# Kernel tuning notes

Hardware: AMD Instinct MI355X
Metric: run time of the kernel (lower is better)

Reference implementation:

```python
import jax, jax.numpy as jnp
import numpy as np

BS, QLEN, DIM, NH = 4, 2048, 1024, 16
DH = DIM // NH
NEG = float(np.finfo(np.float32).min)


def setup_inputs() -> dict:
    key = jax.random.key(0)
    ks = jax.random.split(key, 10)
    s = 1.0 / np.sqrt(DIM)
    return {
        "hidden_states": jax.random.normal(ks[0], (BS, QLEN, DIM), jnp.float32),
        "attention_mask": jnp.ones((BS, QLEN), jnp.int32),
        "Wq": jax.random.normal(ks[1], (DIM, DIM), jnp.float32) * s,
        "bq": jnp.zeros((DIM,), jnp.float32),
        "Wk": jax.random.normal(ks[2], (DIM, DIM), jnp.float32) * s,
        "bk": jnp.zeros((DIM,), jnp.float32),
        "Wv": jax.random.normal(ks[3], (DIM, DIM), jnp.float32) * s,
        "bv": jnp.zeros((DIM,), jnp.float32),
        "Wo": jax.random.normal(ks[4], (DIM, DIM), jnp.float32) * s,
        "bo": jnp.zeros((DIM,), jnp.float32),
    }


def _heads(x, bs):
    # [bs, len, dim] -> [bs, n_heads, len, dim_per_head]
    return x.reshape(bs, -1, NH, DH).transpose(0, 2, 1, 3)


def reference(hidden_states, attention_mask, Wq, bq, Wk, bk, Wv, bv, Wo, bo):
    bs, qlen, dim = hidden_states.shape
    q = _heads(hidden_states @ Wq.T + bq, bs) / jnp.sqrt(jnp.asarray(DH, hidden_states.dtype))
    k = _heads(hidden_states @ Wk.T + bk, bs)
    v = _heads(hidden_states @ Wv.T + bv, bs)
    scores = jnp.einsum("bhqd,bhkd->bhqk", q, k)  # [bs, nh, qlen, klen]
    mask = (attention_mask == 0)[:, None, None, :]  # [bs,1,1,klen]
    scores = jnp.where(mask, NEG, scores)
    weights = jax.nn.softmax(scores.astype(jnp.float32), axis=-1).astype(scores.dtype)
    context = jnp.einsum("bhqk,bhkd->bhqd", weights, v)
    context = context.transpose(0, 2, 1, 3).reshape(bs, qlen, dim)
    return context @ Wo.T + bo
```

## Files before the change

### kernel.cpp

```cpp
#include <hip/hip_runtime.h>
#include <hip/hip_bf16.h>

#define BS 4
#define QLEN 2048
#define DIM 1024
#define NH 16
#define DH 64

typedef __attribute__((ext_vector_type(8))) short bf16x8;
typedef __attribute__((ext_vector_type(4))) float f32x4;
typedef __attribute__((ext_vector_type(16))) float f32x16;
typedef __attribute__((ext_vector_type(2))) unsigned int u32x2;
typedef __attribute__((ext_vector_type(4))) unsigned int u32x4;
typedef unsigned short u16;
typedef unsigned int u32;
typedef unsigned long long u64;

#define LOG2E 1.44269504088896f

__device__ __forceinline__ u32 cvtpk_bf16(float lo, float hi) {
    u32 r;
    asm("v_cvt_pk_bf16_f32 %0, %1, %2" : "=v"(r) : "v"(lo), "v"(hi));
    return r;
}
__device__ __forceinline__ u16 f2bf_hw(float f) { return (u16)cvtpk_bf16(f, f); }

__device__ __forceinline__ void async_lds16(const void* gp, void* lp) {
    __builtin_amdgcn_global_load_lds(
        (const __attribute__((address_space(1))) u32*)(u64)gp,
        (__attribute__((address_space(3))) u32*)(u32)(u64)lp,
        16, 0, 0);
}

__global__ void cvt_fused(const float* __restrict__ H,
                          const float* __restrict__ W0, const float* __restrict__ W1,
                          const float* __restrict__ W2, const float* __restrict__ W3,
                          u16* __restrict__ Hb,
                          u16* __restrict__ D0, u16* __restrict__ D1,
                          u16* __restrict__ D2, u16* __restrict__ D3) {
    const int h4 = (BS * QLEN * DIM) / 4;
    int i = blockIdx.x * blockDim.x + threadIdx.x;
    const float* s;
    u16* d;
    int off;
    if (i < h4) { s = H; d = Hb; off = i; }
    else {
        int j = i - h4;
        int ws = j >> 18;
        off = j & 262143;
        s = ws == 0 ? W0 : ws == 1 ? W1 : ws == 2 ? W2 : W3;
        d = ws == 0 ? D0 : ws == 1 ? D1 : ws == 2 ? D2 : D3;
    }
    float4 v = ((const float4*)s)[off];
    uint2 o;
    o.x = cvtpk_bf16(v.x, v.y);
    o.y = cvtpk_bf16(v.z, v.w);
    ((uint2*)d)[off] = o;
}

__global__ void mask_prep(const int* __restrict__ mask, float* __restrict__ maskF,
                          int* __restrict__ flags) {
    const int tile = blockIdx.x;
    const int lane = threadIdx.x;
    const int idx = tile * 64 + lane;
    const int v = mask[idx];
    maskF[idx] = v ? 1.0f : 0.0f;
    u64 bal = __ballot(v == 0);
    if (lane == 0) flags[tile] = (bal != 0ull) ? 1 : 0;
}

__global__ __launch_bounds__(256) void gemm_qkv(
    const u16* __restrict__ Hb,
    const u16* __restrict__ Wq, const u16* __restrict__ Wk, const u16* __restrict__ Wv,
    const float* __restrict__ bq, const float* __restrict__ bk, const float* __restrict__ bvv,
    u16* __restrict__ Qb, u16* __restrict__ Kb, u16* __restrict__ Vt)
{
    __shared__ __align__(16) u16 As[128 * 32];
    __shared__ __align__(16) u16 Bs[128 * 32];
    const int z = blockIdx.z;
    const u16* W = z == 0 ? Wq : z == 1 ? Wk : Wv;
    const float* bias = z == 0 ? bq : z == 1 ? bk : bvv;
    const int t = threadIdx.x;
    const int w = t >> 6, lane = t & 63;
    const int lr = lane & 15, lg = lane >> 4;
    const int m0 = blockIdx.y * 128, n0 = blockIdx.x * 128;
    const int wm = (w >> 1) * 64, wn = (w & 1) * 64;
    const int srow = w * 16 + (lane >> 2);
    const int sk = (lane & 3) * 8;

    f32x4 acc[4][4] = {};

    for (int kt = 0; kt < DIM; kt += 32) {
        __syncthreads();
        async_lds16(Hb + (u64)(m0 + srow) * DIM + kt + sk,      &As[(w * 16) * 32]);
        async_lds16(Hb + (u64)(m0 + 64 + srow) * DIM + kt + sk, &As[(64 + w * 16) * 32]);
        async_lds16(W + (u64)(n0 + srow) * DIM + kt + sk,       &Bs[(w * 16) * 32]);
        async_lds16(W + (u64)(n0 + 64 + srow) * DIM + kt + sk,  &Bs[(64 + w * 16) * 32]);
        __syncthreads();
        bf16x8 a[4], b[4];
#pragma unroll
        for (int i = 0; i < 4; ++i) a[i] = *(const bf16x8*)&As[(wm + i * 16 + lr) * 32 + lg * 8];
#pragma unroll
        for (int i = 0; i < 4; ++i) b[i] = *(const bf16x8*)&Bs[(wn + i * 16 + lr) * 32 + lg * 8];
#pragma unroll
        for (int mi = 0; mi < 4; ++mi)
#pragma unroll
            for (int ni = 0; ni < 4; ++ni)
                acc[mi][ni] = __builtin_amdgcn_mfma_f32_16x16x32_bf16(a[mi], b[ni], acc[mi][ni], 0, 0, 0);
    }

#pragma unroll
    for (int mi = 0; mi < 4; ++mi)
#pragma unroll
        for (int ni = 0; ni < 4; ++ni) {
            const int col = n0 + wn + ni * 16 + lr;
            const float bb = bias[col];
#pragma unroll
            for (int r = 0; r < 4; ++r) {
                const int row = m0 + wm + mi * 16 + lg * 4 + r;
                const float v = acc[mi][ni][r] + bb;
                const int bh = (row >> 11) * NH + (col >> 6);
                const int q = row & (QLEN - 1);
                const int d = col & (DH - 1);
                if (z == 0)      Qb[((u64)bh * QLEN + q) * DH + d] = f2bf_hw(v * (0.125f * LOG2E));
                else if (z == 1) Kb[((u64)bh * QLEN + q) * DH + d] = f2bf_hw(v);
                else             Vt[((u64)bh * DH + d) * QLEN + q] = f2bf_hw(v);
            }
        }
}

__global__ __launch_bounds__(256) void gemm_o(
    const u16* __restrict__ A, const u16* __restrict__ W,
    const float* __restrict__ bias, float* __restrict__ ofp)
{
    __shared__ __align__(16) u16 As[128 * 32];
    __shared__ __align__(16) u16 Bs[128 * 32];
    const int t = threadIdx.x;
    const int w = t >> 6, lane = t & 63;
    const int lr = lane & 15, lg = lane >> 4;
    const int m0 = blockIdx.y * 128, n0 = blockIdx.x * 128;
    const int wm = (w >> 1) * 64, wn = (w & 1) * 64;
    const int srow = w * 16 + (lane >> 2);
    const int sk = (lane & 3) * 8;

    f32x4 acc[4][4] = {};

    for (int kt = 0; kt < DIM; kt += 32) {
        __syncthreads();
        async_lds16(A + (u64)(m0 + srow) * DIM + kt + sk,      &As[(w * 16) * 32]);
        async_lds16(A + (u64)(m0 + 64 + srow) * DIM + kt + sk, &As[(64 + w * 16) * 32]);
        async_lds16(W + (u64)(n0 + srow) * DIM + kt + sk,      &Bs[(w * 16) * 32]);
        async_lds16(W + (u64)(n0 + 64 + srow) * DIM + kt + sk, &Bs[(64 + w * 16) * 32]);
        __syncthreads();
        bf16x8 a[4], b[4];
#pragma unroll
        for (int i = 0; i < 4; ++i) a[i] = *(const bf16x8*)&As[(wm + i * 16 + lr) * 32 + lg * 8];
#pragma unroll
        for (int i = 0; i < 4; ++i) b[i] = *(const bf16x8*)&Bs[(wn + i * 16 + lr) * 32 + lg * 8];
#pragma unroll
        for (int mi = 0; mi < 4; ++mi)
#pragma unroll
            for (int ni = 0; ni < 4; ++ni)
                acc[mi][ni] = __builtin_amdgcn_mfma_f32_16x16x32_bf16(a[mi], b[ni], acc[mi][ni], 0, 0, 0);
    }

#pragma unroll
    for (int mi = 0; mi < 4; ++mi)
#pragma unroll
        for (int ni = 0; ni < 4; ++ni) {
            const int col = n0 + wn + ni * 16 + lr;
            const float bb = bias[col];
#pragma unroll
            for (int r = 0; r < 4; ++r) {
                const int row = m0 + wm + mi * 16 + lg * 4 + r;
                ofp[(u64)row * DIM + col] = acc[mi][ni][r] + bb;
            }
        }
}

__global__ __launch_bounds__(256, 3) void attn_kernel(
    const u16* __restrict__ Qb, const u16* __restrict__ Kb, const u16* __restrict__ Vt,
    const float* __restrict__ maskF, const int* __restrict__ mflags, u16* __restrict__ ctx)
{
    __shared__ __align__(16) u16 Ks[3][64 * 64];
    __shared__ __align__(16) u16 Vs[3][64 * 64];

    const int t = threadIdx.x;
    const int w = t >> 6, lane = t & 63;
    const int l5 = lane & 31, hi = lane >> 5, l7 = lane & 7;

    const int id = blockIdx.x + 16 * blockIdx.y;
    const int v = (id & 7) * 128 + (id >> 3);
    const int qt = v & 15, bh = v >> 4;
    const int b = bh >> 4, hh = bh & 15;
    const int q0 = qt * 128;

    const u16* Kbh = Kb + (u64)bh * QLEN * DH;
    const u16* Vth = Vt + (u64)bh * DH * QLEN;
    const float* mFb = maskF + b * QLEN;
    const int* flb = mflags + b * (QLEN / 64);

    const u64 fmask = __ballot(flb[lane & 31] != 0);

    const u16* qp = Qb + ((u64)bh * QLEN + q0 + w * 32 + l5) * DH + hi * 8;
    bf16x8 bq[4];
#pragma unroll
    for (int dc = 0; dc < 4; ++dc) bq[dc] = *(const bf16x8*)(qp + dc * 16);

    f32x16 o[2] = {};
    float mrun = -3.0e38f, lsum = 0.f;

    auto STAGE = [&](int B, int KT) {
#pragma unroll
        for (int c = 0; c < 2; ++c) {
            const int row = w * 16 + c * 8 + (lane >> 3);
            const int ch = l7 ^ (row & 7);
            async_lds16(Kbh + (u64)(KT * 64 + row) * DH + ch * 8, &Ks[B][(w * 16 + c * 8) * 64]);
            async_lds16(Vth + (u64)row * QLEN + KT * 64 + ch * 8, &Vs[B][(w * 16 + c * 8) * 64]);
        }
    };

    auto compute = [&](int B, int kt64) {
        const char* Kbase = (const char*)&Ks[B][0];
        const char* Vbase = (const char*)&Vs[B][0];

        f32x16 s[2] = {};
        __builtin_amdgcn_s_setprio(1);
#pragma unroll
        for (int dc = 0; dc < 4; ++dc) {
            const u32 off = (u32)(l5 * 128) + (u32)(((2 * dc + hi) ^ l7) << 4);
            bf16x8 ak0 = *(const bf16x8*)(Kbase + off);
            bf16x8 ak1 = *(const bf16x8*)(Kbase + off + 4096);
            s[0] = __builtin_amdgcn_mfma_f32_32x32x16_bf16(ak0, bq[dc], s[0], 0, 0, 0);
            s[1] = __builtin_amdgcn_mfma_f32_32x32x16_bf16(ak1, bq[dc], s[1], 0, 0, 0);
        }
        __builtin_amdgcn_s_setprio(0);

        bf16x8 av0[4], av1[4];
#pragma unroll
        for (int kc = 0; kc < 4; ++kc) {
            const u32 voff = (u32)(l5 * 128) + (u32)(((2 * kc + hi) ^ l7) << 4);
            av0[kc] = *(const bf16x8*)(Vbase + voff);
            av1[kc] = *(const bf16x8*)(Vbase + voff + 4096);
        }

        float mx[16];
#pragma unroll
        for (int i = 0; i < 16; ++i) mx[i] = fmaxf(s[0][i], s[1][i]);
#pragma unroll
        for (int st = 8; st > 0; st >>= 1)
#pragma unroll
            for (int i = 0; i < 16; ++i) if (i < st) mx[i] = fmaxf(mx[i], mx[i + st]);
        const float tma = fmaxf(mx[0], __shfl_xor(mx[0], 32));

        if (!__all(tma <= mrun + 11.5415603f)) {
            const float nm = fmaxf(mrun, tma);
            const float corr = exp2f(mrun - nm);
            mrun = nm;
            lsum *= corr;
#pragma unroll
            for (int i = 0; i < 16; ++i) { o[0][i] *= corr; o[1][i] *= corr; }
        }

#pragma unroll
        for (int i = 0; i < 16; ++i) {
            s[0][i] = exp2f(s[0][i] - mrun);
            s[1][i] = exp2f(s[1][i] - mrun);
        }

        if ((fmask >> kt64) & 1ull) {
#pragma unroll
            for (int kb = 0; kb < 2; ++kb)
#pragma unroll
                for (int m = 0; m < 4; ++m) {
                    float4 mm = *(const float4*)&mFb[kt64 * 64 + kb * 32 + m * 8 + hi * 4];
                    s[kb][4 * m + 0] *= mm.x;
                    s[kb][4 * m + 1] *= mm.y;
                    s[kb][4 * m + 2] *= mm.z;
                    s[kb][4 * m + 3] *= mm.w;
                }
        }

        {
            float ps[16];
#pragma unroll
            for (int i = 0; i < 16; ++i) ps[i] = s[0][i] + s[1][i];
#pragma unroll
            for (int st = 8; st > 0; st >>= 1)
#pragma unroll
                for (int i = 0; i < 16; ++i) if (i < st) ps[i] += ps[i + st];
            lsum += ps[0];
        }

        __builtin_amdgcn_s_setprio(1);
#pragma unroll
        for (int kc = 0; kc < 4; ++kc) {
            const int kb = kc >> 1;
            const int base = 8 * (kc & 1);
            const u32 P00 = cvtpk_bf16(s[kb][base + 0], s[kb][base + 1]);
            const u32 P01 = cvtpk_bf16(s[kb][base + 2], s[kb][base + 3]);
            const u32 P10 = cvtpk_bf16(s[kb][base + 4], s[kb][base + 5]);
            const u32 P11 = cvtpk_bf16(s[kb][base + 6], s[kb][base + 7]);
            u32x2 w02 = __builtin_amdgcn_permlane32_swap(P00, P10, false, false);
            u32x2 w13 = __builtin_amdgcn_permlane32_swap(P01, P11, false, false);
            u32x4 words;
            words.x = w02[0]; words.y = w13[0]; words.z = w02[1]; words.w = w13[1];
            const bf16x8 bp = __builtin_bit_cast(bf16x8, words);

            o[0] = __builtin_amdgcn_mfma_f32_32x32x16_bf16(av0[kc], bp, o[0], 0, 0, 0);
            o[1] = __builtin_amdgcn_mfma_f32_32x32x16_bf16(av1[kc], bp, o[1], 0, 0, 0);
        }
        __builtin_amdgcn_s_setprio(0);
    };

    STAGE(0, 0);
    STAGE(1, 1);
    int rb = 0, sb = 2;
    for (int tt = 0; tt < 31; ++tt) {
        asm volatile("s_waitcnt vmcnt(4)" ::: "memory");
        __builtin_amdgcn_s_barrier();
        __builtin_amdgcn_sched_barrier(0);
        if (tt + 2 < 32) STAGE(sb, tt + 2);
        compute(rb, tt);
        rb = (rb == 2) ? 0 : rb + 1;
        sb = (sb == 2) ? 0 : sb + 1;
    }
    asm volatile("s_waitcnt vmcnt(0)" ::: "memory");
    __builtin_amdgcn_s_barrier();
    __builtin_amdgcn_sched_barrier(0);
    compute(rb, 31);

    const float lall = lsum + __shfl_xor(lsum, 32);
    const float inv = 1.0f / fmaxf(lall, 1e-37f);

    u16* cp = ctx + (((u64)b * QLEN + (q0 + w * 32 + l5)) * NH + hh) * DH;
#pragma unroll
    for (int db = 0; db < 2; ++db)
#pragma unroll
        for (int m = 0; m < 4; ++m) {
            const int d0 = db * 32 + m * 8 + hi * 4;
            const u32 wA = cvtpk_bf16(o[db][4 * m + 0] * inv, o[db][4 * m + 1] * inv);
            const u32 wB = cvtpk_bf16(o[db][4 * m + 2] * inv, o[db][4 * m + 3] * inv);
            *(u32*)(cp + d0) = wA;
            *(u32*)(cp + d0 + 2) = wB;
        }
}

extern "C" void kernel_launch(void* const* d_in, const int* in_sizes, int n_in,
                              void* d_out, int out_size, void* d_ws, size_t ws_size,
                              hipStream_t stream) {
    const float* H    = (const float*)d_in[0];
    const int*   mask = (const int*)d_in[1];
    const float* Wq   = (const float*)d_in[2];
    const float* bq   = (const float*)d_in[3];
    const float* Wk   = (const float*)d_in[4];
    const float* bk   = (const float*)d_in[5];
    const float* Wv   = (const float*)d_in[6];
    const float* bv   = (const float*)d_in[7];
    const float* Wo   = (const float*)d_in[8];
    const float* bo   = (const float*)d_in[9];
    float* out = (float*)d_out;

    const u64 NTOK = (u64)BS * QLEN;
    const u64 HN = NTOK * DIM;
    const u64 WN = (u64)DIM * DIM;

    u16* Hb  = (u16*)d_ws;
    u16* Wqb = Hb + HN;
    u16* Wkb = Wqb + WN;
    u16* Wvb = Wkb + WN;
    u16* Wob = Wvb + WN;
    u16* Qb  = Wob + WN;
    u16* Kb  = Qb + HN;
    u16* Vtg = Kb + HN;
    u16* Ctx = Vtg + HN;
    float* maskF = (float*)(Ctx + HN);
    int* mflags = (int*)(maskF + BS * QLEN);

    cvt_fused<<<12288, 256, 0, stream>>>(H, Wq, Wk, Wv, Wo, Hb, Wqb, Wkb, Wvb, Wob);
    mask_prep<<<BS * (QLEN / 64), 64, 0, stream>>>(mask, maskF, mflags);

    gemm_qkv<<<dim3(DIM / 128, (int)(NTOK / 128), 3), 256, 0, stream>>>(
        Hb, Wqb, Wkb, Wvb, bq, bk, bv, Qb, Kb, Vtg);

    attn_kernel<<<dim3(QLEN / 128, BS * NH), 256, 0, stream>>>(Qb, Kb, Vtg, maskF, mflags, Ctx);

    gemm_o<<<dim3(DIM / 128, (int)(NTOK / 128)), 256, 0, stream>>>(Ctx, Wob, bo, out);
}
```

Baseline: 247.2 us.

## Widen attention KV tile to 128 keys with double buffering

The attention kernel now processes 128 keys per iteration instead of 64, using two LDS buffers of 128-key K/V tiles in place of three 64-key buffers. The V tile gets a 16-chunk XOR swizzle, and V fragments are loaded from LDS inside the PV loop rather than prefetched. This halves the number of barriers and online-softmax rescale checks per query tile. In exchange it keeps only one tile in flight, waiting with vmcnt(0) each step, and lowers launch-bounds occupancy from 3 to 2 blocks per CU.

```diff
diff --git a/kernel.cpp b/kernel.cpp
--- a/kernel.cpp
+++ b/kernel.cpp
@@ -178,12 +178,12 @@
         }
 }
 
-__global__ __launch_bounds__(256, 3) void attn_kernel(
+__global__ __launch_bounds__(256, 2) void attn_kernel(
     const u16* __restrict__ Qb, const u16* __restrict__ Kb, const u16* __restrict__ Vt,
     const float* __restrict__ maskF, const int* __restrict__ mflags, u16* __restrict__ ctx)
 {
-    __shared__ __align__(16) u16 Ks[3][64 * 64];
-    __shared__ __align__(16) u16 Vs[3][64 * 64];
+    __shared__ __align__(16) u16 Ks[2][128 * 64];
+    __shared__ __align__(16) u16 Vs[2][64 * 128];
 
     const int t = threadIdx.x;
     const int w = t >> 6, lane = t & 63;
@@ -210,43 +210,54 @@
     f32x16 o[2] = {};
     float mrun = -3.0e38f, lsum = 0.f;
 
+    const int krow_l = lane >> 3;
+    const int vrow_l = lane >> 4;
+    const int vslot = lane & 15;
+
     auto STAGE = [&](int B, int KT) {
 #pragma unroll
-        for (int c = 0; c < 2; ++c) {
-            const int row = w * 16 + c * 8 + (lane >> 3);
-            const int ch = l7 ^ (row & 7);
-            async_lds16(Kbh + (u64)(KT * 64 + row) * DH + ch * 8, &Ks[B][(w * 16 + c * 8) * 64]);
-            async_lds16(Vth + (u64)row * QLEN + KT * 64 + ch * 8, &Vs[B][(w * 16 + c * 8) * 64]);
+        for (int c = 0; c < 4; ++c) {
+            const int krow = w * 32 + c * 8 + krow_l;
+            const int kch = l7 ^ (krow & 7);
+            async_lds16(Kbh + (u64)(KT * 128 + krow) * DH + kch * 8,
+                        &Ks[B][(w * 32 + c * 8) * 64]);
+            const int vrow = w * 16 + c * 4 + vrow_l;
+            const int vch = vslot ^ (vrow & 15);
+            async_lds16(Vth + (u64)vrow * QLEN + KT * 128 + vch * 8,
+                        &Vs[B][(w * 16 + c * 4) * 128]);
         }
     };
 
-    auto compute = [&](int B, int kt64) {
+    auto compute = [&](int B, int tt) {
         const char* Kbase = (const char*)&Ks[B][0];
         const char* Vbase = (const char*)&Vs[B][0];
 
-        f32x16 s[2] = {};
+        f32x16 s0 = {}, s1 = {}, s2 = {}, s3 = {};
         __builtin_amdgcn_s_setprio(1);
 #pragma unroll
         for (int dc = 0; dc < 4; ++dc) {
-            const u32 off = (u32)(l5 * 128) + (u32)(((2 * dc + hi) ^ l7) << 4);
-            bf16x8 ak0 = *(const bf16x8*)(Kbase + off);
-            bf16x8 ak1 = *(const bf16x8*)(Kbase + off + 4096);
-            s[0] = __builtin_amdgcn_mfma_f32_32x32x16_bf16(ak0, bq[dc], s[0], 0, 0, 0);
-            s[1] = __builtin_amdgcn_mfma_f32_32x32x16_bf16(ak1, bq[dc], s[1], 0, 0, 0);
+            bf16x8 ak0, ak1, ak2, ak3;
+            {
+                const u32 c = (u32)(2 * dc + hi);
+#pragma unroll
+                for (int kb = 0; kb < 4; ++kb) {
+                    const u32 row = kb * 32 + l5;
+                    const u32 off = row * 128 + ((c ^ (row & 7)) << 4);
+                    bf16x8 a = *(const bf16x8*)(Kbase + off);
+                    if (kb == 0) ak0 = a; else if (kb == 1) ak1 = a;
+                    else if (kb == 2) ak2 = a; else ak3 = a;
+                }
+            }
+            s0 = __builtin_amdgcn_mfma_f32_32x32x16_bf16(ak0, bq[dc], s0, 0, 0, 0);
+            s1 = __builtin_amdgcn_mfma_f32_32x32x16_bf16(ak1, bq[dc], s1, 0, 0, 0);
+            s2 = __builtin_amdgcn_mfma_f32_32x32x16_bf16(ak2, bq[dc], s2, 0, 0, 0);
+            s3 = __builtin_amdgcn_mfma_f32_32x32x16_bf16(ak3, bq[dc], s3, 0, 0, 0);
         }
         __builtin_amdgcn_s_setprio(0);
 
-        bf16x8 av0[4], av1[4];
-#pragma unroll
-        for (int kc = 0; kc < 4; ++kc) {
-            const u32 voff = (u32)(l5 * 128) + (u32)(((2 * kc + hi) ^ l7) << 4);
-            av0[kc] = *(const bf16x8*)(Vbase + voff);
-            av1[kc] = *(const bf16x8*)(Vbase + voff + 4096);
-        }
-
         float mx[16];
 #pragma unroll
-        for (int i = 0; i < 16; ++i) mx[i] = fmaxf(s[0][i], s[1][i]);
+        for (int i = 0; i < 16; ++i) mx[i] = fmaxf(fmaxf(s0[i], s1[i]), fmaxf(s2[i], s3[i]));
 #pragma unroll
         for (int st = 8; st > 0; st >>= 1)
 #pragma unroll
@@ -264,27 +275,31 @@
 
 #pragma unroll
         for (int i = 0; i < 16; ++i) {
-            s[0][i] = exp2f(s[0][i] - mrun);
-            s[1][i] = exp2f(s[1][i] - mrun);
-        }
-
-        if ((fmask >> kt64) & 1ull) {
-#pragma unroll
-            for (int kb = 0; kb < 2; ++kb)
+            s0[i] = exp2f(s0[i] - mrun);
+            s1[i] = exp2f(s1[i] - mrun);
+            s2[i] = exp2f(s2[i] - mrun);
+            s3[i] = exp2f(s3[i] - mrun);
+        }
+
+        if ((fmask >> (2 * tt)) & 3ull) {
+#pragma unroll
+            for (int kb = 0; kb < 4; ++kb) {
+                f32x16& sk = kb == 0 ? s0 : kb == 1 ? s1 : kb == 2 ? s2 : s3;
 #pragma unroll
                 for (int m = 0; m < 4; ++m) {
-                    float4 mm = *(const float4*)&mFb[kt64 * 64 + kb * 32 + m * 8 + hi * 4];
-                    s[kb][4 * m + 0] *= mm.x;
-                    s[kb][4 * m + 1] *= mm.y;
-                    s[kb][4 * m + 2] *= mm.z;
-                    s[kb][4 * m + 3] *= mm.w;
+                    float4 mm = *(const float4*)&mFb[tt * 128 + kb * 32 + m * 8 + hi * 4];
+                    sk[4 * m + 0] *= mm.x;
+                    sk[4 * m + 1] *= mm.y;
+                    sk[4 * m + 2] *= mm.z;
+                    sk[4 * m + 3] *= mm.w;
                 }
+            }
         }
 
         {
             float ps[16];
 #pragma unroll
-            for (int i = 0; i < 16; ++i) ps[i] = s[0][i] + s[1][i];
+            for (int i = 0; i < 16; ++i) ps[i] = (s0[i] + s1[i]) + (s2[i] + s3[i]);
 #pragma unroll
             for (int st = 8; st > 0; st >>= 1)
 #pragma unroll
@@ -294,41 +309,41 @@
 
         __builtin_amdgcn_s_setprio(1);
 #pragma unroll
-        for (int kc = 0; kc < 4; ++kc) {
+        for (int kc = 0; kc < 8; ++kc) {
             const int kb = kc >> 1;
+            const f32x16& sk = kb == 0 ? s0 : kb == 1 ? s1 : kb == 2 ? s2 : s3;
             const int base = 8 * (kc & 1);
-            const u32 P00 = cvtpk_bf16(s[kb][base + 0], s[kb][base + 1]);
-            const u32 P01 = cvtpk_bf16(s[kb][base + 2], s[kb][base + 3]);
-            const u32 P10 = cvtpk_bf16(s[kb][base + 4], s[kb][base + 5]);
-            const u32 P11 = cvtpk_bf16(s[kb][base + 6], s[kb][base + 7]);
+            const u32 P00 = cvtpk_bf16(sk[base + 0], sk[base + 1]);
+            const u32 P01 = cvtpk_bf16(sk[base + 2], sk[base + 3]);
+            const u32 P10 = cvtpk_bf16(sk[base + 4], sk[base + 5]);
+            const u32 P11 = cvtpk_bf16(sk[base + 6], sk[base + 7]);
             u32x2 w02 = __builtin_amdgcn_permlane32_swap(P00, P10, false, false);
             u32x2 w13 = __builtin_amdgcn_permlane32_swap(P01, P11, false, false);
             u32x4 words;
             words.x = w02[0]; words.y = w13[0]; words.z = w02[1]; words.w = w13[1];
             const bf16x8 bp = __builtin_bit_cast(bf16x8, words);
 
-            o[0] = __builtin_amdgcn_mfma_f32_32x32x16_bf16(av0[kc], bp, o[0], 0, 0, 0);
-            o[1] = __builtin_amdgcn_mfma_f32_32x32x16_bf16(av1[kc], bp, o[1], 0, 0, 0);
+            const u32 c = (u32)(2 * kc + hi);
+            const u32 r0 = (u32)l5;
+            const u32 off0 = r0 * 256 + ((c ^ (r0 & 15)) << 4);
+            const u32 r1 = (u32)(32 + l5);
+            const u32 off1 = r1 * 256 + ((c ^ (r1 & 15)) << 4);
+            bf16x8 av0 = *(const bf16x8*)(Vbase + off0);
+            bf16x8 av1 = *(const bf16x8*)(Vbase + off1);
+            o[0] = __builtin_amdgcn_mfma_f32_32x32x16_bf16(av0, bp, o[0], 0, 0, 0);
+            o[1] = __builtin_amdgcn_mfma_f32_32x32x16_bf16(av1, bp, o[1], 0, 0, 0);
         }
         __builtin_amdgcn_s_setprio(0);
     };
 
     STAGE(0, 0);
-    STAGE(1, 1);
-    int rb = 0, sb = 2;
-    for (int tt = 0; tt < 31; ++tt) {
-        asm volatile("s_waitcnt vmcnt(4)" ::: "memory");
+    for (int tt = 0; tt < 16; ++tt) {
+        asm volatile("s_waitcnt vmcnt(0)" ::: "memory");
         __builtin_amdgcn_s_barrier();
         __builtin_amdgcn_sched_barrier(0);
-        if (tt + 2 < 32) STAGE(sb, tt + 2);
-        compute(rb, tt);
-        rb = (rb == 2) ? 0 : rb + 1;
-        sb = (sb == 2) ? 0 : sb + 1;
+        if (tt + 1 < 16) STAGE((tt + 1) & 1, tt + 1);
+        compute(tt & 1, tt);
     }
-    asm volatile("s_waitcnt vmcnt(0)" ::: "memory");
-    __builtin_amdgcn_s_barrier();
-    __builtin_amdgcn_sched_barrier(0);
-    compute(rb, 31);
 
     const float lall = lsum + __shfl_xor(lsum, 32);
     const float inv = 1.0f / fmaxf(lall, 1e-37f);
```

Result: no change. 248.1 us (+0.3%).

## Software-pipeline QK of next tile against softmax/PV of current tile

Applied to the files above, without the earlier changes.

Splits the attention inner step into separate QK and softmax+PV stages. The loop is unrolled by two so the QK MFMAs for tile t+1 are issued before the softmax and PV for tile t, using ping-pong score registers. LDS staging grows from three to four buffers to keep three tiles in flight. The goal is to hide the softmax VALU and exp latency behind matrix-core work. The cost is higher register and LDS use, which lowers launch_bounds occupancy from three to two blocks per CU.

```diff
diff --git a/kernel.cpp b/kernel.cpp
--- a/kernel.cpp
+++ b/kernel.cpp
@@ -178,12 +178,12 @@
         }
 }
 
-__global__ __launch_bounds__(256, 3) void attn_kernel(
+__global__ __launch_bounds__(256, 2) void attn_kernel(
     const u16* __restrict__ Qb, const u16* __restrict__ Kb, const u16* __restrict__ Vt,
     const float* __restrict__ maskF, const int* __restrict__ mflags, u16* __restrict__ ctx)
 {
-    __shared__ __align__(16) u16 Ks[3][64 * 64];
-    __shared__ __align__(16) u16 Vs[3][64 * 64];
+    __shared__ __align__(16) u16 Ks[4][64 * 64];
+    __shared__ __align__(16) u16 Vs[4][64 * 64];
 
     const int t = threadIdx.x;
     const int w = t >> 6, lane = t & 63;
@@ -220,21 +220,24 @@
         }
     };
 
-    auto compute = [&](int B, int kt64) {
+    auto QK = [&](f32x16& s0, f32x16& s1, int B) {
         const char* Kbase = (const char*)&Ks[B][0];
-        const char* Vbase = (const char*)&Vs[B][0];
-
-        f32x16 s[2] = {};
+        s0 = f32x16{};
+        s1 = f32x16{};
         __builtin_amdgcn_s_setprio(1);
 #pragma unroll
         for (int dc = 0; dc < 4; ++dc) {
             const u32 off = (u32)(l5 * 128) + (u32)(((2 * dc + hi) ^ l7) << 4);
             bf16x8 ak0 = *(const bf16x8*)(Kbase + off);
             bf16x8 ak1 = *(const bf16x8*)(Kbase + off + 4096);
-            s[0] = __builtin_amdgcn_mfma_f32_32x32x16_bf16(ak0, bq[dc], s[0], 0, 0, 0);
-            s[1] = __builtin_amdgcn_mfma_f32_32x32x16_bf16(ak1, bq[dc], s[1], 0, 0, 0);
+            s0 = __builtin_amdgcn_mfma_f32_32x32x16_bf16(ak0, bq[dc], s0, 0, 0, 0);
+            s1 = __builtin_amdgcn_mfma_f32_32x32x16_bf16(ak1, bq[dc], s1, 0, 0, 0);
         }
         __builtin_amdgcn_s_setprio(0);
+    };
+
+    auto SMPV = [&](f32x16& s0, f32x16& s1, int B, int kt64) {
+        const char* Vbase = (const char*)&Vs[B][0];
 
         bf16x8 av0[4], av1[4];
 #pragma unroll
@@ -246,7 +249,7 @@
 
         float mx[16];
 #pragma unroll
-        for (int i = 0; i < 16; ++i) mx[i] = fmaxf(s[0][i], s[1][i]);
+        for (int i = 0; i < 16; ++i) mx[i] = fmaxf(s0[i], s1[i]);
 #pragma unroll
         for (int st = 8; st > 0; st >>= 1)
 #pragma unroll
@@ -264,27 +267,29 @@
 
 #pragma unroll
         for (int i = 0; i < 16; ++i) {
-            s[0][i] = exp2f(s[0][i] - mrun);
-            s[1][i] = exp2f(s[1][i] - mrun);
+            s0[i] = exp2f(s0[i] - mrun);
+            s1[i] = exp2f(s1[i] - mrun);
         }
 
         if ((fmask >> kt64) & 1ull) {
 #pragma unroll
-            for (int kb = 0; kb < 2; ++kb)
+            for (int kb = 0; kb < 2; ++kb) {
+                f32x16& sk = kb == 0 ? s0 : s1;
 #pragma unroll
                 for (int m = 0; m < 4; ++m) {
                     float4 mm = *(const float4*)&mFb[kt64 * 64 + kb * 32 + m * 8 + hi * 4];
-                    s[kb][4 * m + 0] *= mm.x;
-                    s[kb][4 * m + 1] *= mm.y;
-                    s[kb][4 * m + 2] *= mm.z;
-                    s[kb][4 * m + 3] *= mm.w;
+                    sk[4 * m + 0] *= mm.x;
+                    sk[4 * m + 1] *= mm.y;
+                    sk[4 * m + 2] *= mm.z;
+                    sk[4 * m + 3] *= mm.w;
                 }
+            }
         }
 
         {
             float ps[16];
 #pragma unroll
-            for (int i = 0; i < 16; ++i) ps[i] = s[0][i] + s[1][i];
+            for (int i = 0; i < 16; ++i) ps[i] = s0[i] + s1[i];
 #pragma unroll
             for (int st = 8; st > 0; st >>= 1)
 #pragma unroll
@@ -295,12 +300,12 @@
         __builtin_amdgcn_s_setprio(1);
 #pragma unroll
         for (int kc = 0; kc < 4; ++kc) {
-            const int kb = kc >> 1;
+            const f32x16& sk = (kc >> 1) == 0 ? s0 : s1;
             const int base = 8 * (kc & 1);
-            const u32 P00 = cvtpk_bf16(s[kb][base + 0], s[kb][base + 1]);
-            const u32 P01 = cvtpk_bf16(s[kb][base + 2], s[kb][base + 3]);
-            const u32 P10 = cvtpk_bf16(s[kb][base + 4], s[kb][base + 5]);
-            const u32 P11 = cvtpk_bf16(s[kb][base + 6], s[kb][base + 7]);
+            const u32 P00 = cvtpk_bf16(sk[base + 0], sk[base + 1]);
+            const u32 P01 = cvtpk_bf16(sk[base + 2], sk[base + 3]);
+            const u32 P10 = cvtpk_bf16(sk[base + 4], sk[base + 5]);
+            const u32 P11 = cvtpk_bf16(sk[base + 6], sk[base + 7]);
             u32x2 w02 = __builtin_amdgcn_permlane32_swap(P00, P10, false, false);
             u32x2 w13 = __builtin_amdgcn_permlane32_swap(P01, P11, false, false);
             u32x4 words;
@@ -313,22 +318,36 @@
         __builtin_amdgcn_s_setprio(0);
     };
 
+    f32x16 sX0, sX1, sY0, sY1;
+
     STAGE(0, 0);
     STAGE(1, 1);
-    int rb = 0, sb = 2;
-    for (int tt = 0; tt < 31; ++tt) {
+    STAGE(2, 2);
+    asm volatile("s_waitcnt vmcnt(8)" ::: "memory");
+    __builtin_amdgcn_s_barrier();
+    __builtin_amdgcn_sched_barrier(0);
+    QK(sX0, sX1, 0);
+
+    for (int tt = 0; tt < 30; tt += 2) {
         asm volatile("s_waitcnt vmcnt(4)" ::: "memory");
         __builtin_amdgcn_s_barrier();
         __builtin_amdgcn_sched_barrier(0);
-        if (tt + 2 < 32) STAGE(sb, tt + 2);
-        compute(rb, tt);
-        rb = (rb == 2) ? 0 : rb + 1;
-        sb = (sb == 2) ? 0 : sb + 1;
+        if (tt + 3 < 32) STAGE((tt + 3) & 3, tt + 3);
+        QK(sY0, sY1, (tt + 1) & 3);
+        SMPV(sX0, sX1, tt & 3, tt);
+        asm volatile("s_waitcnt vmcnt(4)" ::: "memory");
+        __builtin_amdgcn_s_barrier();
+        __builtin_amdgcn_sched_barrier(0);
+        if (tt + 4 < 32) STAGE((tt + 4) & 3, tt + 4);
+        QK(sX0, sX1, (tt + 2) & 3);
+        SMPV(sY0, sY1, (tt + 1) & 3, tt + 1);
     }
     asm volatile("s_waitcnt vmcnt(0)" ::: "memory");
     __builtin_amdgcn_s_barrier();
     __builtin_amdgcn_sched_barrier(0);
-    compute(rb, 31);
+    QK(sY0, sY1, 31 & 3);
+    SMPV(sX0, sX1, 30 & 3, 30);
+    SMPV(sY0, sY1, 31 & 3, 31);
 
     const float lall = lsum + __shfl_xor(lsum, 32);
     const float inv = 1.0f / fmaxf(lall, 1e-37f);
```

Measured after the change: 252.6 us. +2.2%, slower.
